# Optimization experiments

Measured on AMD Instinct MI355X. Metric: run time of the kernel, lower is better.

Reference implementation:

```python
import jax, jax.numpy as jnp
import numpy as np

N_SUB, N_AGR, N_URB = 100000, 200000, 100000
E_SS, E_AS, E_US = 1_600_000, 400_000, 200_000
D_SUB, D_HRU, H, OUT, L = 128, 32, 128, 16, 3


def setup_inputs() -> dict:
    key = jax.random.key(0)
    ks = jax.random.split(key, 20)
    s = 0.05
    inp = {
        "x_sub": jax.random.normal(ks[0], (N_SUB, D_SUB), jnp.float32),
        "x_agr": jax.random.normal(ks[1], (N_AGR, D_HRU), jnp.float32),
        "x_urb": jax.random.normal(ks[2], (N_URB, D_HRU), jnp.float32),
        "ss_src": jax.random.randint(ks[3], (E_SS,), 0, N_SUB, jnp.int32),
        "ss_dst": jax.random.randint(ks[4], (E_SS,), 0, N_SUB, jnp.int32),
        "as_src": jax.random.randint(ks[5], (E_AS,), 0, N_AGR, jnp.int32),
        "as_dst": jax.random.randint(ks[6], (E_AS,), 0, N_SUB, jnp.int32),
        "us_src": jax.random.randint(ks[7], (E_US,), 0, N_URB, jnp.int32),
        "us_dst": jax.random.randint(ks[8], (E_US,), 0, N_SUB, jnp.int32),
        # Stacked per-layer SAGEConv params (in_sub == hidden, so uniform shapes).
        # lin_l (neighbor path, has bias) and lin_r (root path, no bias).
        "Wl_ss": jax.random.normal(ks[9], (L, H, H), jnp.float32) * s,
        "bl_ss": jnp.zeros((L, H), jnp.float32),
        "Wr_ss": jax.random.normal(ks[10], (L, H, H), jnp.float32) * s,
        "Wl_as": jax.random.normal(ks[11], (L, D_HRU, H), jnp.float32) * s,
        "bl_as": jnp.zeros((L, H), jnp.float32),
        "Wr_as": jax.random.normal(ks[12], (L, H, H), jnp.float32) * s,
        "Wl_us": jax.random.normal(ks[13], (L, D_HRU, H), jnp.float32) * s,
        "bl_us": jnp.zeros((L, H), jnp.float32),
        "Wr_us": jax.random.normal(ks[14], (L, H, H), jnp.float32) * s,
        "Wf": jax.random.normal(ks[15], (H, OUT), jnp.float32) * s,
        "bf": jnp.zeros((OUT,), jnp.float32),
    }
    return inp


def reference(x_sub, x_agr, x_urb, ss_src, ss_dst, as_src, as_dst, us_src,
              us_dst, Wl_ss, bl_ss, Wr_ss, Wl_as, bl_as, Wr_as, Wl_us, bl_us,
              Wr_us, Wf, bf):
    # Degree of each sub node under sub->sub edges (for mean aggr, layers>0).
    deg = jax.ops.segment_sum(jnp.ones((E_SS,), x_sub.dtype), ss_dst,
                              num_segments=N_SUB)
    deg = jnp.maximum(deg, 1.0)[:, None]  # [N_SUB,1]

    h = x_sub
    for i in range(L):
        # sub -> sub: gather + scatter-add (sum at layer 0, mean afterwards)
        agg_ss = jax.ops.segment_sum(h[ss_src], ss_dst, num_segments=N_SUB)
        if i > 0:
            agg_ss = agg_ss / deg  # PyG default aggr='mean' for layers > 0
        # hru_agr -> sub and hru_urb -> sub: sum aggregation (sage_aggr='sum')
        agg_as = jax.ops.segment_sum(x_agr[as_src], as_dst, num_segments=N_SUB)
        agg_us = jax.ops.segment_sum(x_urb[us_src], us_dst, num_segments=N_SUB)
        # SAGEConv: lin_l(aggr msgs) + lin_r(x_dst); HeteroConv aggr='sum'.
        out = (agg_ss @ Wl_ss[i] + bl_ss[i] + h @ Wr_ss[i]
               + agg_as @ Wl_as[i] + bl_as[i] + h @ Wr_as[i]
               + agg_us @ Wl_us[i] + bl_us[i] + h @ Wr_us[i])
        h = jax.nn.relu(out)  # norms are Identity; dropout in eval mode
    logits = h @ Wf + bf
    return jax.nn.softmax(logits, axis=1)
```

## Files before the change

kernel.cpp:

```cpp
#include <hip/hip_runtime.h>
#include <hip/hip_bf16.h>

#define N_SUB 100000
#define N_AGR 200000
#define N_URB 100000
#define E_SS  1600000
#define E_AS  400000
#define E_US  200000
#define HID   128
#define DHRU  32
#define NOUT  16
#define NL    3
#define SCAN_T 12500

typedef unsigned short u16;
typedef unsigned int u32;
typedef short bf16x8 __attribute__((ext_vector_type(8)));
typedef float f32x4 __attribute__((ext_vector_type(4)));

static __device__ __forceinline__ u16 f2b(float f) {
    u32 x = __float_as_uint(f);
    u32 r = (x + 0x7fffu + ((x >> 16) & 1u)) >> 16;
    return (u16)r;
}
static __device__ __forceinline__ float blo(u32 u) { return __uint_as_float(u << 16); }
static __device__ __forceinline__ float bhi(u32 u) { return __uint_as_float(u & 0xffff0000u); }


__global__ void hist_kernel(const int* __restrict__ dst, int* __restrict__ deg, int n) {
    int i = blockIdx.x * 256 + threadIdx.x;
    if (i < n) atomicAdd(&deg[dst[i]], 1);
}

__global__ void scan_p1(const int* __restrict__ deg, int* __restrict__ tsum) {
    int i = blockIdx.x * 256 + threadIdx.x;
    if (i >= SCAN_T) return;
    const int4* p = (const int4*)(deg + i * 8);
    int4 a = p[0], b = p[1];
    tsum[i] = a.x + a.y + a.z + a.w + b.x + b.y + b.z + b.w;
}

__global__ void scan_p2(int* __restrict__ tsum) {
    __shared__ int sh[256];
    const int tid = threadIdx.x;
    const int start = tid * 49;
    const int end = min(start + 49, SCAN_T);
    int s = 0;
    for (int i = start; i < end; ++i) s += tsum[i];
    sh[tid] = s;
    __syncthreads();
    for (int o = 1; o < 256; o <<= 1) {
        int t = (tid >= o) ? sh[tid - o] : 0;
        __syncthreads();
        sh[tid] += t;
        __syncthreads();
    }
    int off = (tid > 0) ? sh[tid - 1] : 0;
    for (int i = start; i < end; ++i) {
        int v = tsum[i];
        tsum[i] = off;
        off += v;
    }
}

__global__ void scan_p3(int* __restrict__ degcur, const int* __restrict__ tsum,
                        int* __restrict__ ro, float* inv_deg) {
    int i = blockIdx.x * 256 + threadIdx.x;
    if (i >= SCAN_T) return;
    int off = tsum[i];
#pragma unroll
    for (int j = 0; j < 8; ++j) {
        int idx = i * 8 + j;
        int d = degcur[idx];
        ro[idx] = off;
        if (inv_deg) inv_deg[idx] = 1.0f / (float)(d > 1 ? d : 1);
        degcur[idx] = off;
        off += d;
    }
    if (i == SCAN_T - 1) ro[N_SUB] = off;
}

__global__ void fill_kernel(const int* __restrict__ src, const int* __restrict__ dst,
                            int* __restrict__ cursor, int* __restrict__ csr, int n) {
    int i = blockIdx.x * 256 + threadIdx.x;
    if (i < n) {
        int p = atomicAdd(&cursor[dst[i]], 1);
        csr[p] = src[i];
    }
}

__global__ __launch_bounds__(256)
void agg2_gather(const float* __restrict__ x_agr, const float* __restrict__ x_urb,
                 const int* __restrict__ ro_as, const int* __restrict__ csr_as,
                 const int* __restrict__ ro_us, const int* __restrict__ csr_us,
                 u16* __restrict__ agg2b, int n) {
    int node = blockIdx.x * 4 + (threadIdx.x >> 6);
    int lane = threadIdx.x & 63;
    if (node >= n) return;
    const bool is_us = lane >= 32;
    const int col = lane & 31;
    const int* ro = is_us ? ro_us : ro_as;
    const int* csr = is_us ? csr_us : csr_as;
    const float* x = is_us ? x_urb : x_agr;
    int beg = ro[node], end = ro[node + 1];
    float acc = 0.f;
    for (int p = beg; p < end; ++p) {
        acc += x[(size_t)csr[p] * 32 + col];
    }
    agg2b[(size_t)node * 64 + lane] = f2b(acc);
}

__global__ void add3_kernel(const float* __restrict__ a, const float* __restrict__ b,
                            const float* __restrict__ c, float* __restrict__ o, int n) {
    int i = blockIdx.x * 256 + threadIdx.x;
    if (i < n) o[i] = a[i] + b[i] + c[i];
}

__global__ void build_bp(const float* __restrict__ Wl_ss, const float* __restrict__ Wr_ss,
                         const float* __restrict__ Wr_as, const float* __restrict__ Wr_us,
                         const float* __restrict__ Wl_as, const float* __restrict__ Wl_us,
                         u16* __restrict__ Bp) {
    int b = blockIdx.x;
    int lane = threadIdx.x;
    int lay = b / 80, rem = b % 80, s = rem / 8, c = rem % 8;
    int col = c * 16 + (lane & 15);
    u16* o = Bp + (size_t)(((lay * 80) + s * 8 + c) * 64 + lane) * 8;
#pragma unroll
    for (int j = 0; j < 8; ++j) {
        int k = s * 32 + (lane >> 4) * 8 + j;
        float v;
        if (k < 128) {
            v = Wl_ss[((size_t)lay * 128 + k) * 128 + col];
        } else if (k < 256) {
            size_t idx = ((size_t)lay * 128 + (k - 128)) * 128 + col;
            v = Wr_ss[idx] + Wr_as[idx] + Wr_us[idx];
        } else if (k < 288) {
            v = Wl_as[((size_t)lay * 32 + (k - 256)) * 128 + col];
        } else {
            v = Wl_us[((size_t)lay * 32 + (k - 288)) * 128 + col];
        }
        o[j] = f2b(v);
    }
}

__global__ void cvt_f32_bf16(const float* __restrict__ in, u16* __restrict__ o, int n4) {
    int i = blockIdx.x * 256 + threadIdx.x;
    if (i >= n4) return;
    float4 v = ((const float4*)in)[i];
    ushort4 u;
    u.x = f2b(v.x); u.y = f2b(v.y); u.z = f2b(v.z); u.w = f2b(v.w);
    ((ushort4*)o)[i] = u;
}

__global__ __launch_bounds__(256)
void agg_ss_bf16(const u32* __restrict__ h32, const int* __restrict__ ro,
                 const int* __restrict__ csr, const float* __restrict__ inv_deg,
                 u32* __restrict__ out32, int n, int use_mean) {
    int node = blockIdx.x * 4 + (threadIdx.x >> 6);
    int lane = threadIdx.x & 63;
    if (node >= n) return;
    int beg = ro[node], end = ro[node + 1];
    float a0 = 0.f, a1 = 0.f;
    int p = beg;
    for (; p + 1 < end; p += 2) {
        int s0 = csr[p], s1 = csr[p + 1];
        u32 u0 = h32[(size_t)s0 * 64 + lane];
        u32 u1 = h32[(size_t)s1 * 64 + lane];
        a0 += blo(u0) + blo(u1);
        a1 += bhi(u0) + bhi(u1);
    }
    if (p < end) {
        u32 u0 = h32[(size_t)csr[p] * 64 + lane];
        a0 += blo(u0);
        a1 += bhi(u0);
    }
    if (use_mean) {
        float iv = inv_deg[node];
        a0 *= iv; a1 *= iv;
    }
    out32[(size_t)node * 64 + lane] = (u32)f2b(a0) | ((u32)f2b(a1) << 16);
}

__global__ __launch_bounds__(256)
void layer_gemm_mfma(const u16* __restrict__ agss, const u16* __restrict__ h,
                     const u16* __restrict__ agg2b, const u16* __restrict__ Bp,
                     const float* __restrict__ bsum, u16* __restrict__ out, int n) {
    __shared__ __align__(16) u16 tile[4][32][136];
    const int tid = threadIdx.x;
    const int w = tid >> 6, l = tid & 63;
    const int lr = l & 15, lq = l >> 4;
    const int rows0 = blockIdx.x * 128 + w * 32;

    f32x4 acc[2][8];
#pragma unroll
    for (int rf = 0; rf < 2; ++rf)
#pragma unroll
        for (int c = 0; c < 8; ++c) acc[rf][c] = (f32x4){0.f, 0.f, 0.f, 0.f};

    const bf16x8 zf = {0, 0, 0, 0, 0, 0, 0, 0};

#pragma unroll
    for (int s = 0; s < 10; ++s) {
        const u16* X;
        int ld, koff;
        if (s < 4)      { X = agss;  ld = 128; koff = s * 32 + lq * 8; }
        else if (s < 8) { X = h;     ld = 128; koff = (s - 4) * 32 + lq * 8; }
        else            { X = agg2b; ld = 64;  koff = (s - 8) * 32 + lq * 8; }
        bf16x8 a[2];
#pragma unroll
        for (int rf = 0; rf < 2; ++rf) {
            int row = rows0 + rf * 16 + lr;
            a[rf] = (row < n) ? *(const bf16x8*)(X + (size_t)row * ld + koff) : zf;
        }
        const u16* bp = Bp + ((size_t)(s * 8) * 64 + l) * 8;
#pragma unroll
        for (int c = 0; c < 8; ++c) {
            bf16x8 b = *(const bf16x8*)(bp + (size_t)c * 64 * 8);
            acc[0][c] = __builtin_amdgcn_mfma_f32_16x16x32_bf16(a[0], b, acc[0][c], 0, 0, 0);
            acc[1][c] = __builtin_amdgcn_mfma_f32_16x16x32_bf16(a[1], b, acc[1][c], 0, 0, 0);
        }
    }

    float bias[8];
#pragma unroll
    for (int c = 0; c < 8; ++c) bias[c] = bsum[c * 16 + lr];

#pragma unroll
    for (int rf = 0; rf < 2; ++rf)
#pragma unroll
        for (int c = 0; c < 8; ++c)
#pragma unroll
            for (int r = 0; r < 4; ++r) {
                float v = fmaxf(acc[rf][c][r] + bias[c], 0.f);
                tile[w][rf * 16 + lq * 4 + r][c * 16 + lr] = f2b(v);
            }

#pragma unroll
    for (int i = 0; i < 8; ++i) {
        int row = i * 4 + lq;
        int grow = rows0 + row;
        if (grow < n)
            *(bf16x8*)(out + (size_t)grow * 128 + lr * 8) =
                *(const bf16x8*)&tile[w][row][lr * 8];
    }
}

__global__ __launch_bounds__(256)
void final_kernel(const u32* __restrict__ h32, const float* __restrict__ Wf,
                  const float* __restrict__ bfv, float* __restrict__ out, int n) {
    __shared__ float wsh[HID * NOUT + NOUT];
    for (int i = threadIdx.x; i < HID * NOUT; i += 256) wsh[i] = Wf[i];
    if (threadIdx.x < NOUT) wsh[HID * NOUT + threadIdx.x] = bfv[threadIdx.x];
    __syncthreads();
    int t = blockIdx.x * 256 + threadIdx.x;
    int node = t >> 4, c = t & 15;
    if (node >= n) return;
    const u32* hr = h32 + (size_t)node * 64;
    float acc = wsh[HID * NOUT + c];
#pragma unroll 4
    for (int k2 = 0; k2 < 64; ++k2) {
        u32 u = hr[k2];
        acc += blo(u) * wsh[(2 * k2) * NOUT + c] + bhi(u) * wsh[(2 * k2 + 1) * NOUT + c];
    }
    float m = acc;
#pragma unroll
    for (int o = 8; o >= 1; o >>= 1) m = fmaxf(m, __shfl_xor(m, o, 16));
    float e = expf(acc - m);
    float ssum = e;
#pragma unroll
    for (int o = 8; o >= 1; o >>= 1) ssum += __shfl_xor(ssum, o, 16);
    out[(size_t)node * NOUT + c] = e / ssum;
}

extern "C" void kernel_launch(void* const* d_in, const int* in_sizes, int n_in,
                              void* d_out, int out_size, void* d_ws, size_t ws_size,
                              hipStream_t stream) {
    const float* x_sub = (const float*)d_in[0];
    const float* x_agr = (const float*)d_in[1];
    const float* x_urb = (const float*)d_in[2];
    const int* ss_src = (const int*)d_in[3];
    const int* ss_dst = (const int*)d_in[4];
    const int* as_src = (const int*)d_in[5];
    const int* as_dst = (const int*)d_in[6];
    const int* us_src = (const int*)d_in[7];
    const int* us_dst = (const int*)d_in[8];
    const float* Wl_ss = (const float*)d_in[9];
    const float* bl_ss = (const float*)d_in[10];
    const float* Wr_ss = (const float*)d_in[11];
    const float* Wl_as = (const float*)d_in[12];
    const float* bl_as = (const float*)d_in[13];
    const float* Wr_as = (const float*)d_in[14];
    const float* Wl_us = (const float*)d_in[15];
    const float* bl_us = (const float*)d_in[16];
    const float* Wr_us = (const float*)d_in[17];
    const float* Wf = (const float*)d_in[18];
    const float* bfv = (const float*)d_in[19];
    float* out = (float*)d_out;

    char* ws = (char*)d_ws;
    u16* h0      = (u16*)(ws + 0);
    u16* hA      = (u16*)(ws + 25600000);
    u16* hB      = (u16*)(ws + 51200000);
    u16* agss    = (u16*)(ws + 76800000);
    u16* agg2b   = (u16*)(ws + 102400000);
    float* inv_deg = (float*)(ws + 115200000);
    int* ro_ss   = (int*)(ws + 115600000);
    int* ro_as   = (int*)(ws + 116000016);
    int* ro_us   = (int*)(ws + 116400032);
    int* deg_ss  = (int*)(ws + 116800048);
    int* deg_as  = (int*)(ws + 117200048);
    int* deg_us  = (int*)(ws + 117600048);
    int* csr_ss  = (int*)(ws + 118000048);
    int* csr_as  = (int*)(ws + 124400048);
    int* csr_us  = (int*)(ws + 126000048);
    int* tsum    = (int*)(ws + 126800048);
    u16* Bp      = (u16*)(ws + 126850048);
    float* b_sum = (float*)(ws + 127095808);

    hipMemsetAsync(deg_ss, 0, 3 * N_SUB * sizeof(int), stream);
    hist_kernel<<<(E_SS + 255) / 256, 256, 0, stream>>>(ss_dst, deg_ss, E_SS);
    hist_kernel<<<(E_AS + 255) / 256, 256, 0, stream>>>(as_dst, deg_as, E_AS);
    hist_kernel<<<(E_US + 255) / 256, 256, 0, stream>>>(us_dst, deg_us, E_US);

    const int scan_grid = (SCAN_T + 255) / 256;
    scan_p1<<<scan_grid, 256, 0, stream>>>(deg_ss, tsum);
    scan_p2<<<1, 256, 0, stream>>>(tsum);
    scan_p3<<<scan_grid, 256, 0, stream>>>(deg_ss, tsum, ro_ss, inv_deg);
    scan_p1<<<scan_grid, 256, 0, stream>>>(deg_as, tsum);
    scan_p2<<<1, 256, 0, stream>>>(tsum);
    scan_p3<<<scan_grid, 256, 0, stream>>>(deg_as, tsum, ro_as, nullptr);
    scan_p1<<<scan_grid, 256, 0, stream>>>(deg_us, tsum);
    scan_p2<<<1, 256, 0, stream>>>(tsum);
    scan_p3<<<scan_grid, 256, 0, stream>>>(deg_us, tsum, ro_us, nullptr);

    fill_kernel<<<(E_SS + 255) / 256, 256, 0, stream>>>(ss_src, ss_dst, deg_ss, csr_ss, E_SS);
    fill_kernel<<<(E_AS + 255) / 256, 256, 0, stream>>>(as_src, as_dst, deg_as, csr_as, E_AS);
    fill_kernel<<<(E_US + 255) / 256, 256, 0, stream>>>(us_src, us_dst, deg_us, csr_us, E_US);

    agg2_gather<<<(N_SUB + 3) / 4, 256, 0, stream>>>(x_agr, x_urb, ro_as, csr_as,
                                                     ro_us, csr_us, agg2b, N_SUB);

    build_bp<<<240, 64, 0, stream>>>(Wl_ss, Wr_ss, Wr_as, Wr_us, Wl_as, Wl_us, Bp);
    add3_kernel<<<2, 256, 0, stream>>>(bl_ss, bl_as, bl_us, b_sum, NL * HID);

    cvt_f32_bf16<<<(N_SUB * HID / 4 + 255) / 256, 256, 0, stream>>>(x_sub, h0, N_SUB * HID / 4);

    const int agg_grid = (N_SUB + 3) / 4;
    const int gemm_grid = (N_SUB + 127) / 128;
    const size_t BPL = 40960;

    agg_ss_bf16<<<agg_grid, 256, 0, stream>>>((const u32*)h0, ro_ss, csr_ss, inv_deg, (u32*)agss, N_SUB, 0);
    layer_gemm_mfma<<<gemm_grid, 256, 0, stream>>>(agss, h0, agg2b, Bp + 0 * BPL, b_sum + 0 * HID, hA, N_SUB);

    agg_ss_bf16<<<agg_grid, 256, 0, stream>>>((const u32*)hA, ro_ss, csr_ss, inv_deg, (u32*)agss, N_SUB, 1);
    layer_gemm_mfma<<<gemm_grid, 256, 0, stream>>>(agss, hA, agg2b, Bp + 1 * BPL, b_sum + 1 * HID, hB, N_SUB);

    agg_ss_bf16<<<agg_grid, 256, 0, stream>>>((const u32*)hB, ro_ss, csr_ss, inv_deg, (u32*)agss, N_SUB, 1);
    layer_gemm_mfma<<<gemm_grid, 256, 0, stream>>>(agss, hB, agg2b, Bp + 2 * BPL, b_sum + 2 * HID, hA, N_SUB);

    final_kernel<<<(N_SUB * NOUT + 255) / 256, 256, 0, stream>>>((const u32*)hA, Wf, bfv, out, N_SUB);
}
```

Baseline: 798.4 us.

## Vectorize ss gather, merge CSR build kernels, sort CSR, use fixed-point sums

The sub-sub aggregation now loads 16-byte chunks of each neighbor row and processes four edges in parallel per wave, reducing with cross-lane shuffles. This is meant to raise memory-level parallelism in the dominant gather. The histogram, scan and fill steps for the three edge types are merged into single launches to cut launch overhead. A new per-node odd-even sort orders CSR neighbor lists, and sums are accumulated in 64-bit fixed point for order-independent results. The sort and int64 arithmetic add extra cost.

```diff
diff --git a/kernel.cpp b/kernel.cpp
--- a/kernel.cpp
+++ b/kernel.cpp
@@ -7,6 +7,7 @@
 #define E_SS  1600000
 #define E_AS  400000
 #define E_US  200000
+#define E_TOT 2200000
 #define HID   128
 #define DHRU  32
 #define NOUT  16
@@ -15,8 +16,12 @@
 
 typedef unsigned short u16;
 typedef unsigned int u32;
+typedef long long i64;
 typedef short bf16x8 __attribute__((ext_vector_type(8)));
 typedef float f32x4 __attribute__((ext_vector_type(4)));
+
+#define FIXS 4294967296.0f
+#define FIXR 2.3283064365386963e-10f
 
 static __device__ __forceinline__ u16 f2b(float f) {
     u32 x = __float_as_uint(f);
@@ -25,23 +30,29 @@
 }
 static __device__ __forceinline__ float blo(u32 u) { return __uint_as_float(u << 16); }
 static __device__ __forceinline__ float bhi(u32 u) { return __uint_as_float(u & 0xffff0000u); }
-
-
-__global__ void hist_kernel(const int* __restrict__ dst, int* __restrict__ deg, int n) {
-    int i = blockIdx.x * 256 + threadIdx.x;
-    if (i < n) atomicAdd(&deg[dst[i]], 1);
+static __device__ __forceinline__ i64 fx(float v) { return (i64)(v * FIXS); }
+
+
+__global__ void hist3_kernel(const int* __restrict__ ss_dst, const int* __restrict__ as_dst,
+                             const int* __restrict__ us_dst, int* __restrict__ deg_ss,
+                             int* __restrict__ deg_as, int* __restrict__ deg_us) {
+    int i = blockIdx.x * 256 + threadIdx.x;
+    if (i < E_SS) atomicAdd(&deg_ss[ss_dst[i]], 1);
+    else if (i < E_SS + E_AS) atomicAdd(&deg_as[as_dst[i - E_SS]], 1);
+    else if (i < E_TOT) atomicAdd(&deg_us[us_dst[i - E_SS - E_AS]], 1);
 }
 
 __global__ void scan_p1(const int* __restrict__ deg, int* __restrict__ tsum) {
     int i = blockIdx.x * 256 + threadIdx.x;
-    if (i >= SCAN_T) return;
+    if (i >= 3 * SCAN_T) return;
     const int4* p = (const int4*)(deg + i * 8);
     int4 a = p[0], b = p[1];
     tsum[i] = a.x + a.y + a.z + a.w + b.x + b.y + b.z + b.w;
 }
 
-__global__ void scan_p2(int* __restrict__ tsum) {
+__global__ void scan_p2(int* __restrict__ tsum_all) {
     __shared__ int sh[256];
+    int* tsum = tsum_all + blockIdx.x * SCAN_T;
     const int tid = threadIdx.x;
     const int start = tid * 49;
     const int end = min(start + 49, SCAN_T);
@@ -64,29 +75,70 @@
 }
 
 __global__ void scan_p3(int* __restrict__ degcur, const int* __restrict__ tsum,
-                        int* __restrict__ ro, float* inv_deg) {
-    int i = blockIdx.x * 256 + threadIdx.x;
-    if (i >= SCAN_T) return;
+                        int* __restrict__ ro_ss, int* __restrict__ ro_as,
+                        int* __restrict__ ro_us, float* __restrict__ inv_deg) {
+    int i = blockIdx.x * 256 + threadIdx.x;
+    if (i >= 3 * SCAN_T) return;
+    int seg = i / SCAN_T, li = i - seg * SCAN_T;
+    int* ro = (seg == 0) ? ro_ss : (seg == 1) ? ro_as : ro_us;
     int off = tsum[i];
 #pragma unroll
     for (int j = 0; j < 8; ++j) {
-        int idx = i * 8 + j;
-        int d = degcur[idx];
+        int gidx = i * 8 + j;
+        int idx = li * 8 + j;
+        int d = degcur[gidx];
         ro[idx] = off;
-        if (inv_deg) inv_deg[idx] = 1.0f / (float)(d > 1 ? d : 1);
-        degcur[idx] = off;
+        if (seg == 0) inv_deg[idx] = 1.0f / (float)(d > 1 ? d : 1);
+        degcur[gidx] = off;
         off += d;
     }
-    if (i == SCAN_T - 1) ro[N_SUB] = off;
-}
-
-__global__ void fill_kernel(const int* __restrict__ src, const int* __restrict__ dst,
-                            int* __restrict__ cursor, int* __restrict__ csr, int n) {
-    int i = blockIdx.x * 256 + threadIdx.x;
-    if (i < n) {
-        int p = atomicAdd(&cursor[dst[i]], 1);
-        csr[p] = src[i];
-    }
+    if (li == SCAN_T - 1) ro[N_SUB] = off;
+}
+
+__global__ void fill3_kernel(const int* __restrict__ ss_src, const int* __restrict__ ss_dst,
+                             const int* __restrict__ as_src, const int* __restrict__ as_dst,
+                             const int* __restrict__ us_src, const int* __restrict__ us_dst,
+                             int* __restrict__ cur_ss, int* __restrict__ cur_as,
+                             int* __restrict__ cur_us, int* __restrict__ csr_ss,
+                             int* __restrict__ csr_as, int* __restrict__ csr_us) {
+    int i = blockIdx.x * 256 + threadIdx.x;
+    const int* src; const int* dst; int* cur; int* csr; int e;
+    if (i < E_SS)               { src = ss_src; dst = ss_dst; cur = cur_ss; csr = csr_ss; e = i; }
+    else if (i < E_SS + E_AS)   { src = as_src; dst = as_dst; cur = cur_as; csr = csr_as; e = i - E_SS; }
+    else if (i < E_TOT)         { src = us_src; dst = us_dst; cur = cur_us; csr = csr_us; e = i - E_SS - E_AS; }
+    else return;
+    int p = atomicAdd(&cur[dst[e]], 1);
+    csr[p] = src[e];
+}
+
+__global__ __launch_bounds__(256)
+void sort_csr3(const int* __restrict__ ro_ss, int* __restrict__ csr_ss,
+               const int* __restrict__ ro_as, int* __restrict__ csr_as,
+               const int* __restrict__ ro_us, int* __restrict__ csr_us) {
+    __shared__ int buf[4][64];
+    int gnode = blockIdx.x * 4 + (threadIdx.x >> 6);
+    int lane = threadIdx.x & 63;
+    int w = threadIdx.x >> 6;
+    int seg = gnode / N_SUB;
+    int node = gnode - seg * N_SUB;
+    const int* ro = (seg == 0) ? ro_ss : (seg == 1) ? ro_as : ro_us;
+    int* csr = (seg == 0) ? csr_ss : (seg == 1) ? csr_as : csr_us;
+    int beg = ro[node];
+    int len = ro[node + 1] - beg;
+    int nload = min(len, 64);
+    buf[w][lane] = (lane < nload) ? csr[beg + lane] : 0x7FFFFFFF;
+    for (int r = 0; r < 64; ++r) {
+        __syncthreads();
+        if (lane < 32) {
+            int idx = 2 * lane + (r & 1);
+            if (idx + 1 < 64) {
+                int a = buf[w][idx], b = buf[w][idx + 1];
+                if (b < a) { buf[w][idx] = b; buf[w][idx + 1] = a; }
+            }
+        }
+    }
+    __syncthreads();
+    if (lane < nload) csr[beg + lane] = buf[w][lane];
 }
 
 __global__ __launch_bounds__(256)
@@ -103,11 +155,11 @@
     const int* csr = is_us ? csr_us : csr_as;
     const float* x = is_us ? x_urb : x_agr;
     int beg = ro[node], end = ro[node + 1];
-    float acc = 0.f;
+    i64 acc = 0;
     for (int p = beg; p < end; ++p) {
-        acc += x[(size_t)csr[p] * 32 + col];
-    }
-    agg2b[(size_t)node * 64 + lane] = f2b(acc);
+        acc += fx(x[(size_t)csr[p] * 32 + col]);
+    }
+    agg2b[(size_t)node * 64 + lane] = f2b((float)acc * FIXR);
 }
 
 __global__ void add3_kernel(const float* __restrict__ a, const float* __restrict__ b,
@@ -153,32 +205,50 @@
 }
 
 __global__ __launch_bounds__(256)
-void agg_ss_bf16(const u32* __restrict__ h32, const int* __restrict__ ro,
+void agg_ss_bf16(const u16* __restrict__ h, const int* __restrict__ ro,
                  const int* __restrict__ csr, const float* __restrict__ inv_deg,
-                 u32* __restrict__ out32, int n, int use_mean) {
+                 u16* __restrict__ out, int n, int use_mean) {
     int node = blockIdx.x * 4 + (threadIdx.x >> 6);
+    if (node >= n) return;
     int lane = threadIdx.x & 63;
-    if (node >= n) return;
+    int g = lane >> 4, t = lane & 15;
     int beg = ro[node], end = ro[node + 1];
-    float a0 = 0.f, a1 = 0.f;
+    i64 acc[8] = {0, 0, 0, 0, 0, 0, 0, 0};
     int p = beg;
-    for (; p + 1 < end; p += 2) {
-        int s0 = csr[p], s1 = csr[p + 1];
-        u32 u0 = h32[(size_t)s0 * 64 + lane];
-        u32 u1 = h32[(size_t)s1 * 64 + lane];
-        a0 += blo(u0) + blo(u1);
-        a1 += bhi(u0) + bhi(u1);
-    }
-    if (p < end) {
-        u32 u0 = h32[(size_t)csr[p] * 64 + lane];
-        a0 += blo(u0);
-        a1 += bhi(u0);
-    }
-    if (use_mean) {
-        float iv = inv_deg[node];
-        a0 *= iv; a1 *= iv;
-    }
-    out32[(size_t)node * 64 + lane] = (u32)f2b(a0) | ((u32)f2b(a1) << 16);
+    for (; p + 3 < end; p += 4) {
+        int s = csr[p + g];
+        uint4 q = *(const uint4*)(h + (size_t)s * 128 + t * 8);
+        acc[0] += fx(blo(q.x)); acc[1] += fx(bhi(q.x));
+        acc[2] += fx(blo(q.y)); acc[3] += fx(bhi(q.y));
+        acc[4] += fx(blo(q.z)); acc[5] += fx(bhi(q.z));
+        acc[6] += fx(blo(q.w)); acc[7] += fx(bhi(q.w));
+    }
+    int rem = end - p;
+    if (g < rem) {
+        int s = csr[p + g];
+        uint4 q = *(const uint4*)(h + (size_t)s * 128 + t * 8);
+        acc[0] += fx(blo(q.x)); acc[1] += fx(bhi(q.x));
+        acc[2] += fx(blo(q.y)); acc[3] += fx(bhi(q.y));
+        acc[4] += fx(blo(q.z)); acc[5] += fx(bhi(q.z));
+        acc[6] += fx(blo(q.w)); acc[7] += fx(bhi(q.w));
+    }
+#pragma unroll
+    for (int j = 0; j < 8; ++j) {
+        acc[j] += __shfl_xor(acc[j], 16, 64);
+        acc[j] += __shfl_xor(acc[j], 32, 64);
+    }
+    if (g == 0) {
+        float v[8];
+        float iv = use_mean ? inv_deg[node] : 1.0f;
+#pragma unroll
+        for (int j = 0; j < 8; ++j) v[j] = (float)acc[j] * FIXR * iv;
+        uint4 o;
+        o.x = (u32)f2b(v[0]) | ((u32)f2b(v[1]) << 16);
+        o.y = (u32)f2b(v[2]) | ((u32)f2b(v[3]) << 16);
+        o.z = (u32)f2b(v[4]) | ((u32)f2b(v[5]) << 16);
+        o.w = (u32)f2b(v[6]) | ((u32)f2b(v[7]) << 16);
+        *(uint4*)(out + (size_t)node * 128 + t * 8) = o;
+    }
 }
 
 __global__ __launch_bounds__(256)
@@ -314,28 +384,21 @@
     int* csr_as  = (int*)(ws + 124400048);
     int* csr_us  = (int*)(ws + 126000048);
     int* tsum    = (int*)(ws + 126800048);
-    u16* Bp      = (u16*)(ws + 126850048);
-    float* b_sum = (float*)(ws + 127095808);
+    u16* Bp      = (u16*)(ws + 126950048);
+    float* b_sum = (float*)(ws + 127195808);
 
     hipMemsetAsync(deg_ss, 0, 3 * N_SUB * sizeof(int), stream);
-    hist_kernel<<<(E_SS + 255) / 256, 256, 0, stream>>>(ss_dst, deg_ss, E_SS);
-    hist_kernel<<<(E_AS + 255) / 256, 256, 0, stream>>>(as_dst, deg_as, E_AS);
-    hist_kernel<<<(E_US + 255) / 256, 256, 0, stream>>>(us_dst, deg_us, E_US);
-
-    const int scan_grid = (SCAN_T + 255) / 256;
-    scan_p1<<<scan_grid, 256, 0, stream>>>(deg_ss, tsum);
-    scan_p2<<<1, 256, 0, stream>>>(tsum);
-    scan_p3<<<scan_grid, 256, 0, stream>>>(deg_ss, tsum, ro_ss, inv_deg);
-    scan_p1<<<scan_grid, 256, 0, stream>>>(deg_as, tsum);
-    scan_p2<<<1, 256, 0, stream>>>(tsum);
-    scan_p3<<<scan_grid, 256, 0, stream>>>(deg_as, tsum, ro_as, nullptr);
-    scan_p1<<<scan_grid, 256, 0, stream>>>(deg_us, tsum);
-    scan_p2<<<1, 256, 0, stream>>>(tsum);
-    scan_p3<<<scan_grid, 256, 0, stream>>>(deg_us, tsum, ro_us, nullptr);
-
-    fill_kernel<<<(E_SS + 255) / 256, 256, 0, stream>>>(ss_src, ss_dst, deg_ss, csr_ss, E_SS);
-    fill_kernel<<<(E_AS + 255) / 256, 256, 0, stream>>>(as_src, as_dst, deg_as, csr_as, E_AS);
-    fill_kernel<<<(E_US + 255) / 256, 256, 0, stream>>>(us_src, us_dst, deg_us, csr_us, E_US);
+    hist3_kernel<<<(E_TOT + 255) / 256, 256, 0, stream>>>(ss_dst, as_dst, us_dst,
+                                                          deg_ss, deg_as, deg_us);
+    scan_p1<<<(3 * SCAN_T + 255) / 256, 256, 0, stream>>>(deg_ss, tsum);
+    scan_p2<<<3, 256, 0, stream>>>(tsum);
+    scan_p3<<<(3 * SCAN_T + 255) / 256, 256, 0, stream>>>(deg_ss, tsum, ro_ss, ro_as,
+                                                          ro_us, inv_deg);
+    fill3_kernel<<<(E_TOT + 255) / 256, 256, 0, stream>>>(ss_src, ss_dst, as_src, as_dst,
+                                                          us_src, us_dst, deg_ss, deg_as,
+                                                          deg_us, csr_ss, csr_as, csr_us);
+    sort_csr3<<<(3 * N_SUB) / 4, 256, 0, stream>>>(ro_ss, csr_ss, ro_as, csr_as,
+                                                   ro_us, csr_us);
 
     agg2_gather<<<(N_SUB + 3) / 4, 256, 0, stream>>>(x_agr, x_urb, ro_as, csr_as,
                                                      ro_us, csr_us, agg2b, N_SUB);
@@ -349,14 +412,18 @@
     const int gemm_grid = (N_SUB + 127) / 128;
     const size_t BPL = 40960;
 
-    agg_ss_bf16<<<agg_grid, 256, 0, stream>>>((const u32*)h0, ro_ss, csr_ss, inv_deg, (u32*)agss, N_SUB, 0);
-    layer_gemm_mfma<<<gemm_grid, 256, 0, stream>>>(agss, h0, agg2b, Bp + 0 * BPL, b_sum + 0 * HID, hA, N_SUB);
-
-    agg_ss_bf16<<<agg_grid, 256, 0, stream>>>((const u32*)hA, ro_ss, csr_ss, inv_deg, (u32*)agss, N_SUB, 1);
-    layer_gemm_mfma<<<gemm_grid, 256, 0, stream>>>(agss, hA, agg2b, Bp + 1 * BPL, b_sum + 1 * HID, hB, N_SUB);
-
-    agg_ss_bf16<<<agg_grid, 256, 0, stream>>>((const u32*)hB, ro_ss, csr_ss, inv_deg, (u32*)agss, N_SUB, 1);
-    layer_gemm_mfma<<<gemm_grid, 256, 0, stream>>>(agss, hB, agg2b, Bp + 2 * BPL, b_sum + 2 * HID, hA, N_SUB);
-
-    final_kernel<<<(N_SUB * NOUT + 255) / 256, 256, 0, stream>>>((const u32*)hA, Wf, bfv, out, N_SUB);
-}
+    agg_ss_bf16<<<agg_grid, 256, 0, stream>>>(h0, ro_ss, csr_ss, inv_deg, agss, N_SUB, 0);
+    layer_gemm_mfma<<<gemm_grid, 256, 0, stream>>>(agss, h0, agg2b, Bp + 0 * BPL,
+                                                   b_sum + 0 * HID, hA, N_SUB);
+
+    agg_ss_bf16<<<agg_grid, 256, 0, stream>>>(hA, ro_ss, csr_ss, inv_deg, agss, N_SUB, 1);
+    layer_gemm_mfma<<<gemm_grid, 256, 0, stream>>>(agss, hA, agg2b, Bp + 1 * BPL,
+                                                   b_sum + 1 * HID, hB, N_SUB);
+
+    agg_ss_bf16<<<agg_grid, 256, 0, stream>>>(hB, ro_ss, csr_ss, inv_deg, agss, N_SUB, 1);
+    layer_gemm_mfma<<<gemm_grid, 256, 0, stream>>>(agss, hB, agg2b, Bp + 2 * BPL,
+                                                   b_sum + 2 * HID, hA, N_SUB);
+
+    final_kernel<<<(N_SUB * NOUT + 255) / 256, 256, 0, stream>>>((const u32*)hA, Wf, bfv,
+                                                                 out, N_SUB);
+}
```

Result: slower. 1.099 ms (+37.6%).
